# Performance work log

Measured on AMD Instinct MI355X. Metric: run time of the kernel, lower is better.

The kernel has to match this reference:

```python
import jax, jax.numpy as jnp
import numpy as np

N_EMBEDDING = 32
HEAD_SIZE = 64
B, T = 8, 4096


def setup_inputs() -> dict:
    key = jax.random.key(0)
    kx, kk, kq, kv = jax.random.split(key, 4)
    x = jax.random.normal(kx, (B, T, N_EMBEDDING), dtype=jnp.float32)
    Wk = jax.random.normal(kk, (N_EMBEDDING, HEAD_SIZE), dtype=jnp.float32) * 0.05
    Wq = jax.random.normal(kq, (N_EMBEDDING, HEAD_SIZE), dtype=jnp.float32) * 0.05
    Wv = jax.random.normal(kv, (N_EMBEDDING, HEAD_SIZE), dtype=jnp.float32) * 0.05
    return {"x": x, "Wk": Wk, "Wq": Wq, "Wv": Wv}


def reference(x, Wk, Wq, Wv):
    # x: [B, T, C]; projections (no bias)
    k = jnp.einsum("btc,cd->btd", x, Wk)  # [B,T,D]
    q = jnp.einsum("btc,cd->btd", x, Wq)
    v = jnp.einsum("btc,cd->btd", x, Wv)
    # raw scores (NOTE: original module applies no 1/sqrt(D) scaling)
    wei = jnp.einsum("bqd,bkd->bqk", q, k)  # [B,T,T]
    t = x.shape[1]
    causal = jnp.tril(jnp.ones((t, t), dtype=bool))
    wei = jnp.where(causal[None, :, :], wei, -jnp.inf)
    wei = jax.nn.softmax(wei, axis=-1)
    out = jnp.einsum("bqk,bkd->bqd", wei, v)  # [B,T,D]
    return out
```

## Files before the change

### kernel.cpp

```cpp
#include <hip/hip_runtime.h>
#include <hip/hip_bf16.h>

constexpr int Bc = 8;
constexpr int Tt = 4096;
constexpr int Dd = 64;

typedef __attribute__((ext_vector_type(8))) short short8;
typedef __attribute__((ext_vector_type(4))) float floatx4;
typedef __attribute__((ext_vector_type(4))) __fp16 half4;
typedef __attribute__((ext_vector_type(2))) __fp16 half2v;
typedef uint4   __attribute__((may_alias)) uint4_a;
typedef short8  __attribute__((may_alias)) short8_a;
typedef ushort4 __attribute__((may_alias)) ushort4_a;
typedef float4  __attribute__((may_alias)) float4_a;
typedef half4   __attribute__((may_alias)) half4_a;

#define MFMA16(A, B, C)  __builtin_amdgcn_mfma_f32_16x16x32_bf16(A, B, C, 0, 0, 0)
#define MFMAH16(A, B, C) __builtin_amdgcn_mfma_f32_16x16x16f16(A, B, C, 0, 0, 0)
constexpr float LOG2E = 1.4426950408889634f;

constexpr size_t XB_OFF = 0;
constexpr size_t YB_OFF = (size_t)2 << 20;
constexpr size_t XT_OFF = (size_t)4 << 20;
constexpr size_t WV_OFF = (size_t)6 << 20;

__device__ __forceinline__ unsigned rnd16(float x) {
    unsigned u; __builtin_memcpy(&u, &x, 4); return u + 0x8000u;
}
__device__ __forceinline__ unsigned pk_bf2(float lo, float hi) {
    return __builtin_amdgcn_perm(rnd16(hi), rnd16(lo), 0x07060302);
}
__device__ __forceinline__ ushort4 pack4(floatx4 d) {
    union { unsigned u[2]; ushort4 v; } r;
    r.u[0] = pk_bf2(d[0], d[1]);
    r.u[1] = pk_bf2(d[2], d[3]);
    return r.v;
}
__device__ __forceinline__ short8 cvt8(float4 a, float4 b) {
    union { unsigned u[4]; short8 s; } r;
    r.u[0] = pk_bf2(a.x, a.y);
    r.u[1] = pk_bf2(a.z, a.w);
    r.u[2] = pk_bf2(b.x, b.y);
    r.u[3] = pk_bf2(b.z, b.w);
    return r.s;
}

__global__ __launch_bounds__(256) void prep_kernel(
    const float* __restrict__ x,
    const float* __restrict__ Wk, const float* __restrict__ Wq,
    const float* __restrict__ Wv,
    char* __restrict__ ws)
{
    __shared__ uint4 sG[128];
    __shared__ float sX[2048];

    const int bi = blockIdx.x;
    const int b = bi >> 6, ch = bi & 63;
    const int tid = threadIdx.x;
    const int wave = tid >> 6, lane = tid & 63;
    const int ln15 = lane & 15, quad = lane >> 4;
    const size_t bT = (size_t)b * Tt;
    const int r0 = ch * 64;

    const int lr = wave * 16 + ln15;
    const float* xp = x + (bT + r0 + lr) * 32 + quad * 8;
    float4 pX0 = ((const float4_a*)xp)[0];
    float4 pX1 = ((const float4_a*)xp)[1];
    *(float4_a*)(&sX[lr * 32 + quad * 8])     = pX0;
    *(float4_a*)(&sX[lr * 32 + quad * 8 + 4]) = pX1;

    if (wave == 0) {
        floatx4 gC[2][2];
        #pragma unroll
        for (int mt = 0; mt < 2; ++mt)
            #pragma unroll
            for (int nt = 0; nt < 2; ++nt) gC[mt][nt] = (floatx4){0.f,0.f,0.f,0.f};
        #pragma unroll
        for (int kt = 0; kt < 2; ++kt) {
            short8 aG[2], bG[2];
            #pragma unroll
            for (int mt = 0; mt < 2; ++mt) {
                const float* qp = Wq + (ln15 + 16*mt)*64 + 32*kt + quad*8;
                float4 a = ((const float4_a*)qp)[0], bb = ((const float4_a*)qp)[1];
                a.x*=LOG2E; a.y*=LOG2E; a.z*=LOG2E; a.w*=LOG2E;
                bb.x*=LOG2E; bb.y*=LOG2E; bb.z*=LOG2E; bb.w*=LOG2E;
                aG[mt] = cvt8(a, bb);
                const float* kp = Wk + (ln15 + 16*mt)*64 + 32*kt + quad*8;
                bG[mt] = cvt8(((const float4_a*)kp)[0], ((const float4_a*)kp)[1]);
            }
            #pragma unroll
            for (int mt = 0; mt < 2; ++mt)
                #pragma unroll
                for (int nt = 0; nt < 2; ++nt)
                    gC[mt][nt] = MFMA16(aG[mt], bG[nt], gC[mt][nt]);
        }
        unsigned short* sGh = (unsigned short*)sG;
        #pragma unroll
        for (int mt = 0; mt < 2; ++mt)
            #pragma unroll
            for (int nt = 0; nt < 2; ++nt)
                *(ushort4_a*)(sGh + (16*nt + ln15)*32 + 16*mt + quad*4)
                    = pack4(gC[mt][nt]);
    }
    __syncthreads();

    union { unsigned u[4]; uint4 v; } xu;
    xu.u[0] = pk_bf2(pX0.x, pX0.y); xu.u[1] = pk_bf2(pX0.z, pX0.w);
    xu.u[2] = pk_bf2(pX1.x, pX1.y); xu.u[3] = pk_bf2(pX1.z, pX1.w);
    *(uint4_a*)(ws + XB_OFF + (size_t)(bT + r0 + lr) * 64 + quad * 16) = xu.v;

    {
        short8 xq = cvt8(pX0, pX1);
        unsigned short* yb = (unsigned short*)(ws + YB_OFF);
        #pragma unroll
        for (int mt = 0; mt < 2; ++mt) {
            union { uint4 u; short8 s; } g;
            g.u = sG[(16*mt + ln15)*4 + quad];
            floatx4 d = (floatx4){0.f,0.f,0.f,0.f};
            d = MFMA16(g.s, xq, d);
            *(ushort4_a*)(yb + (size_t)(bT + r0 + lr) * 32 + 16*mt + quad*4)
                = pack4(d);
        }
    }

    {
        const int kc = tid >> 6;
        const int c = (tid >> 1) & 31, kh = tid & 1;
        float v[8];
        #pragma unroll
        for (int j = 0; j < 8; ++j) v[j] = sX[(kc*16 + kh*8 + j)*32 + c];
        union { unsigned u[4]; uint4 q; } x4;
        #pragma unroll
        for (int j = 0; j < 4; ++j) {
            union { half2v h; unsigned u; } p;
            p.h = __builtin_amdgcn_cvt_pkrtz(v[2*j], v[2*j+1]);
            x4.u[j] = p.u;
        }
        *(uint4_a*)(ws + XT_OFF
                    + ((size_t)((b*256 + ch*4 + kc) * 32 + c)) * 32 + kh * 16)
            = x4.q;
    }

    if (bi == 0 && wave == 2) {
        const int d = lane;
        unsigned short* wvb = (unsigned short*)(ws + WV_OFF);
        float v[32];
        #pragma unroll
        for (int c2 = 0; c2 < 32; ++c2) v[c2] = Wv[c2*64 + d];
        #pragma unroll
        for (int i2 = 0; i2 < 16; ++i2)
            ((unsigned*)(wvb + d*32))[i2] = pk_bf2(v[2*i2], v[2*i2+1]);
    }
}

__global__ __launch_bounds__(1024, 4) void attn_kernel(
    const char* __restrict__ ws, float* __restrict__ out)
{
    __shared__ float sZ[3 * 2048];
    __shared__ float sL[3 * 256];
    __shared__ uint4 sB[256];

    const int b  = blockIdx.x & 7;
    const int pr = blockIdx.x >> 3;
    const int tid = threadIdx.x;
    const int wave = tid >> 6, lane = tid & 63;
    const int kg = wave >> 2, gw = wave & 3;
    const int ln15 = lane & 15, quad = lane >> 4;
    const size_t bT = (size_t)b * Tt;

    const char* xbB = ws + XB_OFF + bT * 64;
    const char* xtB = ws + XT_OFF + (size_t)b * (256 * 1024);
    const int aOff = ln15 * 64 + quad * 16;
    const int xOff = ln15 * 32 + quad * 8;

    for (int phase = 0; phase < 2; ++phase) {
        const int qt = phase ? pr : 63 - pr;
        const int q0 = qt * 64;
        const int qrow = q0 + gw * 16 + ln15;

        short8 bq;
        {
            union { uint4 u; short8 s; } t0;
            t0.u = *(const uint4_a*)(ws + YB_OFF + (size_t)(bT + qrow) * 64
                                     + quad * 16);
            bq = t0.s;
        }

        floatx4 z4[2];
        z4[0] = (floatx4){0.f,0.f,0.f,0.f};
        z4[1] = (floatx4){0.f,0.f,0.f,0.f};
        float l_lane = 0.f;

        short8 aA[4], aB4[4];

        auto LDA = [&](int k, short8* a) {
            const char* p = xbB + (size_t)k * 4096 + aOff;
            #pragma unroll
            for (int t = 0; t < 4; ++t)
                a[t] = *(const short8_a*)(p + t * 1024);
        };

        auto BODY = [&](int kt, const short8* a) {
            const char* px = xtB + (size_t)kt * 4096 + xOff;
            half4 xa[8];
            #pragma unroll
            for (int t = 0; t < 4; ++t) {
                xa[2*t]   = *(const half4_a*)(px + t * 1024);
                xa[2*t+1] = *(const half4_a*)(px + t * 1024 + 512);
            }
            floatx4 s4[4];
            #pragma unroll
            for (int t = 0; t < 4; ++t) {
                floatx4 c0 = (floatx4){0.f,0.f,0.f,0.f};
                s4[t] = MFMA16(a[t], bq, c0);
            }
            if (kt == qt) {
                #pragma unroll
                for (int t = 0; t < 4; ++t) {
                    const int keyb = kt*64 + 16*t + quad*4;
                    #pragma unroll
                    for (int r = 0; r < 4; ++r) {
                        float p = (keyb + r <= qrow)
                                  ? __builtin_amdgcn_exp2f(s4[t][r]) : 0.f;
                        s4[t][r] = p; l_lane += p;
                    }
                }
            } else {
                #pragma unroll
                for (int t = 0; t < 4; ++t)
                    #pragma unroll
                    for (int r = 0; r < 4; ++r) {
                        float p = __builtin_amdgcn_exp2f(s4[t][r]);
                        s4[t][r] = p; l_lane += p;
                    }
            }
            #pragma unroll
            for (int t = 0; t < 4; ++t) {
                union { half2v h2[2]; half4 h4; } pb;
                pb.h2[0] = __builtin_amdgcn_cvt_pkrtz(s4[t][0], s4[t][1]);
                pb.h2[1] = __builtin_amdgcn_cvt_pkrtz(s4[t][2], s4[t][3]);
                z4[0] = MFMAH16(xa[2*t],   pb.h4, z4[0]);
                z4[1] = MFMAH16(xa[2*t+1], pb.h4, z4[1]);
            }
        };

        int kt = kg;
        if (kt <= qt) {
            LDA(kt, aA);
            while (true) {
                int kn = kt + 4;
                LDA(kn <= qt ? kn : kt, aB4);
                BODY(kt, aA);
                if (kn > qt) break;
                kt = kn; kn = kt + 4;
                LDA(kn <= qt ? kn : kt, aA);
                BODY(kt, aB4);
                if (kn > qt) break;
                kt = kn;
            }
        }

        __syncthreads();
        const int li = gw * 64 + lane;
        if (kg != 0) {
            sL[(kg - 1) * 256 + li] = l_lane;
            float4* zp = (float4*)(sZ + (kg - 1) * 2048);
            zp[li*2 + 0] = make_float4(z4[0][0], z4[0][1], z4[0][2], z4[0][3]);
            zp[li*2 + 1] = make_float4(z4[1][0], z4[1][1], z4[1][2], z4[1][3]);
        }
        __syncthreads();
        if (kg == 0) {
            float l = l_lane + sL[li] + sL[256 + li] + sL[512 + li];
            #pragma unroll
            for (int g = 0; g < 3; ++g) {
                const float4* zp = (const float4*)(sZ + g * 2048);
                float4 za = zp[li*2 + 0], zb2 = zp[li*2 + 1];
                z4[0][0]+=za.x;  z4[0][1]+=za.y;  z4[0][2]+=za.z;  z4[0][3]+=za.w;
                z4[1][0]+=zb2.x; z4[1][1]+=zb2.y; z4[1][2]+=zb2.z; z4[1][3]+=zb2.w;
            }
            l += __shfl_xor(l, 16);
            l += __shfl_xor(l, 32);
            const float inv = 1.f / l;
            const unsigned short* wvb = (const unsigned short*)(ws + WV_OFF);
            short8 wv_f[4];
            #pragma unroll
            for (int t = 0; t < 4; ++t) {
                union { uint4 u; short8 s; } w0;
                w0.u = *(const uint4_a*)(wvb + (16*t + ln15) * 32 + quad * 8);
                wv_f[t] = w0.s;
            }
            unsigned short* sZb = (unsigned short*)sB;
            #pragma unroll
            for (int mt = 0; mt < 2; ++mt)
                *(ushort4_a*)(sZb + (gw*16 + ln15)*32 + 16*mt + quad*4)
                    = pack4(z4[mt]);
            union { uint4 u; short8 s; } zb;
            zb.u = sB[(gw*16 + ln15)*4 + quad];
            #pragma unroll
            for (int t = 0; t < 4; ++t) {
                floatx4 o = (floatx4){0.f,0.f,0.f,0.f};
                o = MFMA16(wv_f[t], zb.s, o);
                *(float4_a*)(out + (bT + (size_t)qrow) * Dd + 16*t + quad*4)
                    = make_float4(o[0]*inv, o[1]*inv, o[2]*inv, o[3]*inv);
            }
        }
        __syncthreads();
    }
}

extern "C" void kernel_launch(void* const* d_in, const int* in_sizes, int n_in,
                              void* d_out, int out_size, void* d_ws, size_t ws_size,
                              hipStream_t stream)
{
    const float* x  = (const float*)d_in[0];
    const float* Wk = (const float*)d_in[1];
    const float* Wq = (const float*)d_in[2];
    const float* Wv = (const float*)d_in[3];
    float* out = (float*)d_out;

    prep_kernel<<<512, 256, 0, stream>>>(x, Wk, Wq, Wv, (char*)d_ws);
    attn_kernel<<<Bc * 32, 1024, 0, stream>>>((const char*)d_ws, out);
}
```

Measured before the change: 101.0 us.

## Process both query tiles concurrently with per-wave 64-row query blocking

The attention kernel no longer runs the two paired query tiles in sequential phases; each half of a 512-thread block handles one tile simultaneously. Each wave now computes all four 16-row query subtiles against its key tiles, so the key and x fragments it loads are reused four times, and the cross-wave reduction is split so every wave finalizes one subtile. This cuts global and L2 loads per unit of work and removes the per-phase barriers. In exchange it raises register pressure (four accumulator sets) and halves the threads per block, which may lower occupancy or latency hiding. The two halves also carry unequal causal work within a block.

Result: faster. 85.58 us (-15.3%).

```diff
diff --git a/kernel.cpp b/kernel.cpp
--- a/kernel.cpp
+++ b/kernel.cpp
@@ -153,68 +153,75 @@
     }
 }
 
-__global__ __launch_bounds__(1024, 4) void attn_kernel(
+__global__ __launch_bounds__(512, 2) void attn_kernel(
     const char* __restrict__ ws, float* __restrict__ out)
 {
-    __shared__ float sZ[3 * 2048];
-    __shared__ float sL[3 * 256];
-    __shared__ uint4 sB[256];
-
-    const int b  = blockIdx.x & 7;
-    const int pr = blockIdx.x >> 3;
+    __shared__ float4 sZm[2][4][4][2][64];
+    __shared__ float  sLm[2][4][4][64];
+    __shared__ uint4  sB4[8][64];
+
+    const int b = blockIdx.x & 7;
+    const int u = blockIdx.x >> 3;
     const int tid = threadIdx.x;
     const int wave = tid >> 6, lane = tid & 63;
-    const int kg = wave >> 2, gw = wave & 3;
+    const int h = wave >> 2, kg = wave & 3;
     const int ln15 = lane & 15, quad = lane >> 4;
     const size_t bT = (size_t)b * Tt;
+
+    const int qt = h ? u : (63 - u);
+    const int q0 = qt * 64;
 
     const char* xbB = ws + XB_OFF + bT * 64;
     const char* xtB = ws + XT_OFF + (size_t)b * (256 * 1024);
     const int aOff = ln15 * 64 + quad * 16;
     const int xOff = ln15 * 32 + quad * 8;
 
-    for (int phase = 0; phase < 2; ++phase) {
-        const int qt = phase ? pr : 63 - pr;
-        const int q0 = qt * 64;
-        const int qrow = q0 + gw * 16 + ln15;
-
-        short8 bq;
-        {
-            union { uint4 u; short8 s; } t0;
-            t0.u = *(const uint4_a*)(ws + YB_OFF + (size_t)(bT + qrow) * 64
-                                     + quad * 16);
-            bq = t0.s;
-        }
-
-        floatx4 z4[2];
-        z4[0] = (floatx4){0.f,0.f,0.f,0.f};
-        z4[1] = (floatx4){0.f,0.f,0.f,0.f};
-        float l_lane = 0.f;
-
-        short8 aA[4], aB4[4];
-
-        auto LDA = [&](int k, short8* a) {
-            const char* p = xbB + (size_t)k * 4096 + aOff;
-            #pragma unroll
-            for (int t = 0; t < 4; ++t)
-                a[t] = *(const short8_a*)(p + t * 1024);
-        };
-
-        auto BODY = [&](int kt, const short8* a) {
-            const char* px = xtB + (size_t)kt * 4096 + xOff;
-            half4 xa[8];
-            #pragma unroll
-            for (int t = 0; t < 4; ++t) {
-                xa[2*t]   = *(const half4_a*)(px + t * 1024);
-                xa[2*t+1] = *(const half4_a*)(px + t * 1024 + 512);
-            }
+    short8 bq[4];
+    #pragma unroll
+    for (int nt = 0; nt < 4; ++nt) {
+        union { uint4 u4; short8 s; } t0;
+        t0.u4 = *(const uint4_a*)(ws + YB_OFF
+                 + (size_t)(bT + q0 + 16*nt + ln15) * 64 + quad * 16);
+        bq[nt] = t0.s;
+    }
+
+    floatx4 z4[4][2];
+    float lq[4];
+    #pragma unroll
+    for (int nt = 0; nt < 4; ++nt) {
+        z4[nt][0] = (floatx4){0.f,0.f,0.f,0.f};
+        z4[nt][1] = (floatx4){0.f,0.f,0.f,0.f};
+        lq[nt] = 0.f;
+    }
+
+    short8 aA[4], aB4[4];
+
+    auto LDA = [&](int k, short8* a) {
+        const char* p = xbB + (size_t)k * 4096 + aOff;
+        #pragma unroll
+        for (int t = 0; t < 4; ++t)
+            a[t] = *(const short8_a*)(p + t * 1024);
+    };
+
+    auto BODY = [&](int kt, const short8* a) {
+        const char* px = xtB + (size_t)kt * 4096 + xOff;
+        half4 xa[8];
+        #pragma unroll
+        for (int t = 0; t < 4; ++t) {
+            xa[2*t]   = *(const half4_a*)(px + t * 1024);
+            xa[2*t+1] = *(const half4_a*)(px + t * 1024 + 512);
+        }
+        __builtin_amdgcn_sched_barrier(0);
+        #pragma unroll
+        for (int nt = 0; nt < 4; ++nt) {
             floatx4 s4[4];
             #pragma unroll
             for (int t = 0; t < 4; ++t) {
                 floatx4 c0 = (floatx4){0.f,0.f,0.f,0.f};
-                s4[t] = MFMA16(a[t], bq, c0);
+                s4[t] = MFMA16(a[t], bq[nt], c0);
             }
             if (kt == qt) {
+                const int qrow = q0 + 16*nt + ln15;
                 #pragma unroll
                 for (int t = 0; t < 4; ++t) {
                     const int keyb = kt*64 + 16*t + quad*4;
@@ -222,7 +229,7 @@
                     for (int r = 0; r < 4; ++r) {
                         float p = (keyb + r <= qrow)
                                   ? __builtin_amdgcn_exp2f(s4[t][r]) : 0.f;
-                        s4[t][r] = p; l_lane += p;
+                        s4[t][r] = p; lq[nt] += p;
                     }
                 }
             } else {
@@ -231,7 +238,7 @@
                     #pragma unroll
                     for (int r = 0; r < 4; ++r) {
                         float p = __builtin_amdgcn_exp2f(s4[t][r]);
-                        s4[t][r] = p; l_lane += p;
+                        s4[t][r] = p; lq[nt] += p;
                     }
             }
             #pragma unroll
@@ -239,72 +246,78 @@
                 union { half2v h2[2]; half4 h4; } pb;
                 pb.h2[0] = __builtin_amdgcn_cvt_pkrtz(s4[t][0], s4[t][1]);
                 pb.h2[1] = __builtin_amdgcn_cvt_pkrtz(s4[t][2], s4[t][3]);
-                z4[0] = MFMAH16(xa[2*t],   pb.h4, z4[0]);
-                z4[1] = MFMAH16(xa[2*t+1], pb.h4, z4[1]);
+                z4[nt][0] = MFMAH16(xa[2*t],   pb.h4, z4[nt][0]);
+                z4[nt][1] = MFMAH16(xa[2*t+1], pb.h4, z4[nt][1]);
             }
-        };
-
-        int kt = kg;
-        if (kt <= qt) {
-            LDA(kt, aA);
-            while (true) {
-                int kn = kt + 4;
-                LDA(kn <= qt ? kn : kt, aB4);
-                BODY(kt, aA);
-                if (kn > qt) break;
-                kt = kn; kn = kt + 4;
-                LDA(kn <= qt ? kn : kt, aA);
-                BODY(kt, aB4);
-                if (kn > qt) break;
-                kt = kn;
-            }
-        }
-
-        __syncthreads();
-        const int li = gw * 64 + lane;
-        if (kg != 0) {
-            sL[(kg - 1) * 256 + li] = l_lane;
-            float4* zp = (float4*)(sZ + (kg - 1) * 2048);
-            zp[li*2 + 0] = make_float4(z4[0][0], z4[0][1], z4[0][2], z4[0][3]);
-            zp[li*2 + 1] = make_float4(z4[1][0], z4[1][1], z4[1][2], z4[1][3]);
-        }
-        __syncthreads();
-        if (kg == 0) {
-            float l = l_lane + sL[li] + sL[256 + li] + sL[512 + li];
-            #pragma unroll
-            for (int g = 0; g < 3; ++g) {
-                const float4* zp = (const float4*)(sZ + g * 2048);
-                float4 za = zp[li*2 + 0], zb2 = zp[li*2 + 1];
-                z4[0][0]+=za.x;  z4[0][1]+=za.y;  z4[0][2]+=za.z;  z4[0][3]+=za.w;
-                z4[1][0]+=zb2.x; z4[1][1]+=zb2.y; z4[1][2]+=zb2.z; z4[1][3]+=zb2.w;
-            }
-            l += __shfl_xor(l, 16);
-            l += __shfl_xor(l, 32);
-            const float inv = 1.f / l;
-            const unsigned short* wvb = (const unsigned short*)(ws + WV_OFF);
-            short8 wv_f[4];
-            #pragma unroll
-            for (int t = 0; t < 4; ++t) {
-                union { uint4 u; short8 s; } w0;
-                w0.u = *(const uint4_a*)(wvb + (16*t + ln15) * 32 + quad * 8);
-                wv_f[t] = w0.s;
-            }
-            unsigned short* sZb = (unsigned short*)sB;
-            #pragma unroll
-            for (int mt = 0; mt < 2; ++mt)
-                *(ushort4_a*)(sZb + (gw*16 + ln15)*32 + 16*mt + quad*4)
-                    = pack4(z4[mt]);
-            union { uint4 u; short8 s; } zb;
-            zb.u = sB[(gw*16 + ln15)*4 + quad];
-            #pragma unroll
-            for (int t = 0; t < 4; ++t) {
-                floatx4 o = (floatx4){0.f,0.f,0.f,0.f};
-                o = MFMA16(wv_f[t], zb.s, o);
-                *(float4_a*)(out + (bT + (size_t)qrow) * Dd + 16*t + quad*4)
-                    = make_float4(o[0]*inv, o[1]*inv, o[2]*inv, o[3]*inv);
-            }
-        }
-        __syncthreads();
+        }
+    };
+
+    int kt = kg;
+    if (kt <= qt) {
+        LDA(kt, aA);
+        while (true) {
+            int kn = kt + 4;
+            LDA(kn <= qt ? kn : kt, aB4);
+            BODY(kt, aA);
+            if (kn > qt) break;
+            kt = kn; kn = kt + 4;
+            LDA(kn <= qt ? kn : kt, aA);
+            BODY(kt, aB4);
+            if (kn > qt) break;
+            kt = kn;
+        }
+    }
+
+    #pragma unroll
+    for (int nt = 0; nt < 4; ++nt) {
+        sZm[h][nt][kg][0][lane] = make_float4(z4[nt][0][0], z4[nt][0][1],
+                                              z4[nt][0][2], z4[nt][0][3]);
+        sZm[h][nt][kg][1][lane] = make_float4(z4[nt][1][0], z4[nt][1][1],
+                                              z4[nt][1][2], z4[nt][1][3]);
+        sLm[h][nt][kg][lane] = lq[nt];
+    }
+    __syncthreads();
+
+    {
+        const int nt = kg;
+        float4 zm0 = make_float4(0.f,0.f,0.f,0.f);
+        float4 zm1 = make_float4(0.f,0.f,0.f,0.f);
+        float l = 0.f;
+        #pragma unroll
+        for (int g = 0; g < 4; ++g) {
+            float4 a0 = sZm[h][nt][g][0][lane];
+            float4 a1 = sZm[h][nt][g][1][lane];
+            zm0.x+=a0.x; zm0.y+=a0.y; zm0.z+=a0.z; zm0.w+=a0.w;
+            zm1.x+=a1.x; zm1.y+=a1.y; zm1.z+=a1.z; zm1.w+=a1.w;
+            l += sLm[h][nt][g][lane];
+        }
+        l += __shfl_xor(l, 16);
+        l += __shfl_xor(l, 32);
+        const float inv = 1.f / l;
+
+        const unsigned short* wvb = (const unsigned short*)(ws + WV_OFF);
+        short8 wv_f[4];
+        #pragma unroll
+        for (int t = 0; t < 4; ++t) {
+            union { uint4 u4; short8 s; } w0;
+            w0.u4 = *(const uint4_a*)(wvb + (16*t + ln15) * 32 + quad * 8);
+            wv_f[t] = w0.s;
+        }
+        unsigned short* sZb = (unsigned short*)&sB4[wave][0];
+        floatx4 zv0 = (floatx4){zm0.x, zm0.y, zm0.z, zm0.w};
+        floatx4 zv1 = (floatx4){zm1.x, zm1.y, zm1.z, zm1.w};
+        *(ushort4_a*)(sZb + ln15*32 + quad*4)      = pack4(zv0);
+        *(ushort4_a*)(sZb + ln15*32 + 16 + quad*4) = pack4(zv1);
+        union { uint4 u4; short8 s; } zb;
+        zb.u4 = sB4[wave][ln15*4 + quad];
+        const int qrow = q0 + 16*nt + ln15;
+        #pragma unroll
+        for (int t = 0; t < 4; ++t) {
+            floatx4 o = (floatx4){0.f,0.f,0.f,0.f};
+            o = MFMA16(wv_f[t], zb.s, o);
+            *(float4_a*)(out + (bT + (size_t)qrow) * Dd + 16*t + quad*4)
+                = make_float4(o[0]*inv, o[1]*inv, o[2]*inv, o[3]*inv);
+        }
     }
 }
 
@@ -319,5 +332,5 @@
     float* out = (float*)d_out;
 
     prep_kernel<<<512, 256, 0, stream>>>(x, Wk, Wq, Wv, (char*)d_ws);
-    attn_kernel<<<Bc * 32, 1024, 0, stream>>>((const char*)d_ws, out);
-}
+    attn_kernel<<<Bc * 32, 512, 0, stream>>>((const char*)d_ws, out);
+}
```
